# Optimization experiments

Measured on AMD Instinct MI355X. Metric: run time of the kernel, lower is better.

Reference implementation:

```python
import jax, jax.numpy as jnp
import numpy as np

SQRT_2_OVER_PI = 0.7978845608028654

def gelu_tanh(x):
    return 0.5 * x * (1.0 + jnp.tanh(SQRT_2_OVER_PI * (x + 0.044715 * x ** 3)))

def setup_inputs() -> dict:
    key = jax.random.key(0)
    ks = jax.random.split(key, 16)
    B, L, H, Dk, Dv = 4, 512, 8, 64, 64
    dm = H * Dk
    inp = {
        'q': jax.random.normal(ks[0], (B, L, dm), jnp.float32),
        'k': jax.random.normal(ks[1], (B, L, dm), jnp.float32),
        'v': jax.random.normal(ks[2], (B, L, dm), jnp.float32),
        'vec_adj_k': jax.random.normal(ks[3], (B, L, L, Dk), jnp.float32),
        'vec_adj_v': jax.random.normal(ks[4], (B, L, L, Dv), jnp.float32),
        'adj_k': jax.random.randint(ks[5], (B, L, L), 0, 2, jnp.int32),
        'adj_v': jax.random.randint(ks[6], (B, L, L), 0, 2, jnp.int32),
        # learned params (Linear weights stored as [in, out]; y = x @ W)
        'w_qs': jax.random.normal(ks[7], (dm, H * Dk), jnp.float32) * 0.02,
        'w_ks': jax.random.normal(ks[8], (dm, H * Dk), jnp.float32) * 0.02,
        'w_vs': jax.random.normal(ks[9], (dm, H * Dv), jnp.float32) * 0.02,
        'w_fc': jax.random.normal(ks[10], (H * Dk, H * Dk), jnp.float32) * 0.02,
        'w_nw': jax.random.normal(ks[11], (H * Dk, 1), jnp.float32) * 0.02,
        'w_self': jax.random.normal(ks[12], (H * Dk, H * Dk), jnp.float32) * 0.02,
        'w_dd': jax.random.normal(ks[13], (H * Dk, H * Dk), jnp.float32) * 0.02,
    }
    return inp

def reference(q, k, v, vec_adj_k, vec_adj_v, adj_k, adj_v,
              w_qs, w_ks, w_vs, w_fc, w_nw, w_self, w_dd):
    H, Dk, Dv = 8, 64, 64
    B, L, dm = q.shape
    temperature = Dk ** 0.5
    residual = q
    # projections -> [B, H, L, D]
    qh = (q @ w_qs).reshape(B, L, H, Dk).transpose(0, 2, 1, 3)
    kh = (k @ w_ks).reshape(B, L, H, Dk).transpose(0, 2, 1, 3)
    vh = (v @ w_vs).reshape(B, L, H, Dv).transpose(0, 2, 1, 3)
    qs = qh / temperature
    # inner_(q, k, vec_adj_k, flag=True): content + relative-position scores
    scores = jnp.einsum('bhld,bhmd->bhlm', qs, kh) \
           + jnp.einsum('bhld,blmd->bhlm', qs, vec_adj_k)  # [B,H,L,L]
    # adjacency mask (mask == 0 -> -10000)
    scores = jnp.where(adj_k[:, None, :, :] == 0, jnp.float32(-10000.0), scores)
    attn = jax.nn.softmax(scores, axis=-1)
    # inner_(attn, v, vec_adj_v, flag=False)
    out = jnp.einsum('bhlm,bhmd->bhld', attn, vh) \
        + jnp.einsum('bhlm,blmd->bhld', attn, vec_adj_v)
    qc = out.transpose(0, 2, 1, 3).reshape(B, L, H * Dv)  # [B,L,dm]
    # masked neighbor aggregation (GNN stage)
    adj_f = adj_k.astype(qc.dtype)
    nn_num = adj_f.sum(-1)                                  # [B,L]
    denom = jnp.where(nn_num >= 1.0, nn_num, 1.0)
    node_weight = jax.nn.sigmoid((qc @ w_nw)[..., 0])       # [B,L]
    self_info = qc @ w_self
    dd_info = qc @ w_dd
    dd_weight = node_weight[:, None, :] * adj_f             # [B,L,L]
    agg = jnp.matmul(dd_weight, dd_info) / denom[..., None]
    qo = gelu_tanh((self_info + agg) @ w_fc)
    qo = residual + qo
    return (qo, attn)
```

## Files before the change

kernel.cpp:

```cpp
#include <hip/hip_runtime.h>
#include <cstdint>


typedef __attribute__((ext_vector_type(8))) short short8;
typedef __attribute__((ext_vector_type(4))) float f32x4;

__device__ __forceinline__ unsigned short f2bf(float f){
  union { float f; unsigned u; } v; v.f = f;
  unsigned r = (v.u + 0x7fffu + ((v.u >> 16) & 1u)) >> 16;
  return (unsigned short)r;
}

__device__ __forceinline__ short8 ld8(const unsigned short* p){
  return *(const short8*)p;
}

__device__ __forceinline__ f32x4 mfma16(short8 a, short8 b, f32x4 c){
  return __builtin_amdgcn_mfma_f32_16x16x32_bf16(a, b, c, 0, 0, 0);
}

__device__ __forceinline__ float gelu_tanh(float x){
  float u = 0.7978845608028654f * (x + 0.044715f * x * x * x);
  return 0.5f * x * (1.f + tanhf(u));
}

__device__ __forceinline__ short8 pack8(float4 f0, float4 f1){
  short8 s;
  s[0] = (short)f2bf(f0.x); s[1] = (short)f2bf(f0.y);
  s[2] = (short)f2bf(f0.z); s[3] = (short)f2bf(f0.w);
  s[4] = (short)f2bf(f1.x); s[5] = (short)f2bf(f1.y);
  s[6] = (short)f2bf(f1.z); s[7] = (short)f2bf(f1.w);
  return s;
}

template<int LDA, int LDB, int KSTEPS>
__device__ __forceinline__ void gemm64(const unsigned short* __restrict__ A,
                                       const unsigned short* __restrict__ Bp,
                                       f32x4 acc[4][4]){
#pragma unroll 2
  for (int ks = 0; ks < KSTEPS; ks++){
    int kk = ks * 32;
    short8 a[4], b[4];
#pragma unroll
    for (int i = 0; i < 4; i++){
      a[i] = ld8(A + (size_t)i * 16 * LDA + kk);
      b[i] = ld8(Bp + (size_t)i * 16 * LDB + kk);
    }
#pragma unroll
    for (int i = 0; i < 4; i++)
#pragma unroll
      for (int j = 0; j < 4; j++)
        acc[i][j] = mfma16(a[i], b[j], acc[i][j]);
  }
}

__global__ __launch_bounds__(256) void k_prep(const float* __restrict__ q,
    const float* __restrict__ k, const float* __restrict__ v,
    unsigned short* __restrict__ xin,
    const float* __restrict__ wqs, const float* __restrict__ wks,
    const float* __restrict__ wvs, const float* __restrict__ wself,
    const float* __restrict__ wdd, const float* __restrict__ wfc,
    unsigned short* __restrict__ Wt){
  int blk = blockIdx.x;
  int t = threadIdx.x;
  if (blk < 3072){
    int i = blk * 256 + t;
    int w = i >> 18, r = i & 262143;
    const float* src = (w == 0) ? q : (w == 1) ? k : v;
    float4 f = *(const float4*)(src + (size_t)r * 4);
    unsigned lo = (unsigned)f2bf(f.x) | ((unsigned)f2bf(f.y) << 16);
    unsigned hi = (unsigned)f2bf(f.z) | ((unsigned)f2bf(f.w) << 16);
    uint2 o; o.x = lo; o.y = hi;
    *(uint2*)(xin + (size_t)w * 1048576 + (size_t)r * 4) = o;
  } else {
    int i = (blk - 3072) * 256 + t;
    int w = i >> 13;
    int rr = i & 8191;
    int kg = rr >> 9;
    int n  = rr & 511;
    int k0 = kg * 32;
    const float* src = (w == 0) ? wqs : (w == 1) ? wks : (w == 2) ? wvs :
                       (w == 3) ? wself : (w == 4) ? wdd : wfc;
    unsigned pk[16];
#pragma unroll
    for (int j = 0; j < 16; j++){
      float a = src[(size_t)(k0 + 2 * j) * 512 + n];
      float b = src[(size_t)(k0 + 2 * j + 1) * 512 + n];
      pk[j] = (unsigned)f2bf(a) | ((unsigned)f2bf(b) << 16);
    }
    uint4* o4 = (uint4*)(Wt + (size_t)w * 262144 + (size_t)n * 512 + k0);
    o4[0] = make_uint4(pk[0],  pk[1],  pk[2],  pk[3]);
    o4[1] = make_uint4(pk[4],  pk[5],  pk[6],  pk[7]);
    o4[2] = make_uint4(pk[8],  pk[9],  pk[10], pk[11]);
    o4[3] = make_uint4(pk[12], pk[13], pk[14], pk[15]);
  }
}

__global__ __launch_bounds__(256) void k_proj(const unsigned short* __restrict__ xin,
    const unsigned short* __restrict__ Wt, unsigned short* __restrict__ qsb,
    unsigned short* __restrict__ khb, unsigned short* __restrict__ vhT){
  int wid = blockIdx.x * 4 + (threadIdx.x >> 6);
  int mode = wid >> 8;
  int tile = wid & 255;
  int tm = tile >> 3, tn = tile & 7;
  int lane = threadIdx.x & 63;
  int r = lane & 15, qq = lane >> 4;
  const unsigned short* X = xin + (size_t)mode * 1048576;
  const unsigned short* W = Wt + (size_t)mode * 262144;
  unsigned short* dst = (mode == 0) ? qsb : (mode == 1) ? khb : vhT;
  const unsigned short* A  = X + (size_t)(tm * 64 + r) * 512 + qq * 8;
  const unsigned short* Bp = W + (size_t)(tn * 64 + r) * 512 + qq * 8;
  f32x4 acc[4][4] = {};
  gemm64<512, 512, 16>(A, Bp, acc);
  float scv = (mode == 0) ? 0.125f : 1.0f;
  int h = tn;
#pragma unroll
  for (int i = 0; i < 4; i++)
#pragma unroll
    for (int j = 0; j < 4; j++)
#pragma unroll
      for (int e = 0; e < 4; e++){
        int row = tm * 64 + i * 16 + qq * 4 + e;
        int d = j * 16 + r;
        int bb = row >> 9, l = row & 511;
        unsigned short val = f2bf(acc[i][j][e] * scv);
        size_t idx = (mode == 2) ? ((size_t)((bb * 8 + h) * 64 + d) * 512 + l)
                                 : ((size_t)((bb * 8 + h) * 512 + l) * 64 + d);
        dst[idx] = val;
      }
}

__global__ __launch_bounds__(256) void k_scores(const unsigned short* __restrict__ qs,
    const unsigned short* __restrict__ kh, float* __restrict__ attnF){
  int wid = blockIdx.x * 4 + (threadIdx.x >> 6);
  int bh = wid >> 6;
  int tile = wid & 63;
  int tm = tile >> 3, tn = tile & 7;
  int lane = threadIdx.x & 63;
  int r = lane & 15, qq = lane >> 4;
  const unsigned short* A  = qs + (size_t)bh * 32768 + (size_t)(tm * 64 + r) * 64 + qq * 8;
  const unsigned short* Bp = kh + (size_t)bh * 32768 + (size_t)(tn * 64 + r) * 64 + qq * 8;
  f32x4 acc[4][4] = {};
  gemm64<64, 64, 2>(A, Bp, acc);
  float* C = attnF + (size_t)bh * 262144;
#pragma unroll
  for (int i = 0; i < 4; i++)
#pragma unroll
    for (int j = 0; j < 4; j++)
#pragma unroll
      for (int e = 0; e < 4; e++){
        int row = tm * 64 + i * 16 + qq * 4 + e;
        int col = tn * 64 + j * 16 + r;
        C[(size_t)row * 512 + col] = acc[i][j][e];
      }
}

__global__ __launch_bounds__(256) void k_relsoft(const unsigned short* __restrict__ qs,
    const float* __restrict__ vak, const int* __restrict__ adj,
    float* __restrict__ attnF, unsigned short* __restrict__ attn_bf){
  int bid = blockIdx.x;
  int b = bid >> 9, l = bid & 511;
  int t = threadIdx.x, lane = t & 63, w = t >> 6;
  __shared__ __align__(16) unsigned short qsA[16 * 64];
  __shared__ float sc[8 * 512];
  __shared__ int adjs[512];
  for (int j = 0; j < 4; j++){
    int e = t + j * 256;
    int m = e >> 6, d = e & 63;
    qsA[e] = (m < 8) ? qs[((size_t)((b * 8 + m) * 512 + l)) * 64 + d] : (unsigned short)0;
  }
  for (int j = 0; j < 16; j++){
    int e = t + j * 256;
    int h = e >> 9, m = e & 511;
    sc[e] = attnF[((size_t)(b * 8 + h) * 512 + l) * 512 + m];
  }
  adjs[t]       = adj[(size_t)bid * 512 + t];
  adjs[t + 256] = adj[(size_t)bid * 512 + t + 256];
  __syncthreads();
  int r = lane & 15, qq = lane >> 4;
  short8 a0 = ld8(qsA + r * 64 + qq * 8);
  short8 a1 = ld8(qsA + r * 64 + 32 + qq * 8);
  const float* vrow = vak + (size_t)bid * 32768;
#pragma unroll
  for (int c = 0; c < 4; c++){
#pragma unroll
    for (int nt2 = 0; nt2 < 2; nt2++){
      int nt = w * 2 + nt2;
      int m0 = c * 128 + nt * 16 + r;
      const float* p = vrow + (size_t)m0 * 64 + qq * 8;
      float4 f0 = *(const float4*)(p);
      float4 f1 = *(const float4*)(p + 4);
      float4 f2 = *(const float4*)(p + 32);
      float4 f3 = *(const float4*)(p + 36);
      f32x4 acc = {0.f, 0.f, 0.f, 0.f};
      acc = mfma16(a0, pack8(f0, f1), acc);
      acc = mfma16(a1, pack8(f2, f3), acc);
      if (qq < 2){
#pragma unroll
        for (int i = 0; i < 4; i++){
          int h = qq * 4 + i;
          sc[h * 512 + c * 128 + nt * 16 + r] += acc[i];
        }
      }
    }
  }
  __syncthreads();
  for (int hh = 0; hh < 2; hh++){
    int h = w * 2 + hh;
    float v[8]; float mx = -3.0e38f;
    for (int i = 0; i < 8; i++){
      int m = lane + i * 64;
      float s = sc[h * 512 + m];
      if (adjs[m] == 0) s = -10000.0f;
      v[i] = s; mx = fmaxf(mx, s);
    }
    for (int off = 32; off; off >>= 1) mx = fmaxf(mx, __shfl_xor(mx, off, 64));
    float sum = 0.f;
    for (int i = 0; i < 8; i++){ v[i] = __expf(v[i] - mx); sum += v[i]; }
    for (int off = 32; off; off >>= 1) sum += __shfl_xor(sum, off, 64);
    float inv = 1.f / sum;
    size_t base = ((size_t)(b * 8 + h) * 512 + l) * 512;
    for (int i = 0; i < 8; i++){
      int m = lane + i * 64;
      float p2 = v[i] * inv;
      attnF[base + m] = p2;
      attn_bf[base + m] = f2bf(p2);
    }
  }
}

__global__ __launch_bounds__(256) void k_outc(const unsigned short* __restrict__ attn_bf,
    const unsigned short* __restrict__ vhT, float* __restrict__ qc){
  int wid = blockIdx.x * 4 + (threadIdx.x >> 6);
  int bh = wid >> 3;
  int tm = wid & 7;
  int lane = threadIdx.x & 63;
  int r = lane & 15, qq = lane >> 4;
  const unsigned short* A  = attn_bf + (size_t)bh * 262144 + (size_t)(tm * 64 + r) * 512 + qq * 8;
  const unsigned short* Bp = vhT + (size_t)bh * 32768 + (size_t)r * 512 + qq * 8;
  f32x4 acc[4][4] = {};
  gemm64<512, 512, 16>(A, Bp, acc);
  int b = bh >> 3, h = bh & 7;
#pragma unroll
  for (int i = 0; i < 4; i++)
#pragma unroll
    for (int j = 0; j < 4; j++)
#pragma unroll
      for (int e = 0; e < 4; e++){
        int lrow = tm * 64 + i * 16 + qq * 4 + e;
        int d = j * 16 + r;
        qc[(size_t)(b * 512 + lrow) * 512 + h * 64 + d] = acc[i][j][e];
      }
}

__global__ __launch_bounds__(256) void k_outrel(const unsigned short* __restrict__ attn_bf,
    const float* __restrict__ vav, const float* __restrict__ qc,
    const int* __restrict__ adj, const float* __restrict__ wnw,
    unsigned short* __restrict__ qc_bf, float* __restrict__ nw, float* __restrict__ invden){
  int bid = blockIdx.x;
  int b = bid >> 9, l = bid & 511;
  int t = threadIdx.x, lane = t & 63, w = t >> 6;
  __shared__ float orL[512];
  __shared__ float redf[4];
  __shared__ int redi[4];
  int r = lane & 15, qq = lane >> 4;
  int h8 = r & 7;
  const float* vrow = vav + (size_t)bid * 32768;
  const unsigned short* arow = attn_bf + ((size_t)(b * 8 + h8) * 512 + l) * 512;
  f32x4 acc = {0.f, 0.f, 0.f, 0.f};
  int dcol = w * 16 + r;
#pragma unroll
  for (int c = 0; c < 4; c++){
#pragma unroll
    for (int s = 0; s < 4; s++){
      int kk = c * 128 + s * 32;
      short8 av = ld8(arow + kk + qq * 8);
      float fv[8];
#pragma unroll
      for (int j = 0; j < 8; j++)
        fv[j] = vrow[(size_t)(kk + qq * 8 + j) * 64 + dcol];
      short8 bv;
#pragma unroll
      for (int j = 0; j < 8; j++) bv[j] = (short)f2bf(fv[j]);
      acc = mfma16(av, bv, acc);
    }
  }
  if (qq < 2){
#pragma unroll
    for (int i = 0; i < 4; i++){
      int h = qq * 4 + i;
      orL[h * 64 + dcol] = acc[i];
    }
  }
  __syncthreads();
  float part = 0.f; int asum = 0;
  for (int j = 0; j < 2; j++){
    int e = t + j * 256;
    float val = qc[(size_t)bid * 512 + e] + orL[e];
    qc_bf[(size_t)bid * 512 + e] = f2bf(val);
    part += val * wnw[e];
    asum += adj[(size_t)bid * 512 + e];
  }
  for (int off = 32; off; off >>= 1){
    part += __shfl_xor(part, off, 64);
    asum += __shfl_xor(asum, off, 64);
  }
  if (lane == 0){ redf[w] = part; redi[w] = asum; }
  __syncthreads();
  if (t == 0){
    float tot = redf[0] + redf[1] + redf[2] + redf[3];
    int at = redi[0] + redi[1] + redi[2] + redi[3];
    nw[bid] = 1.f / (1.f + __expf(-tot));
    invden[bid] = 1.f / ((at >= 1) ? (float)at : 1.f);
  }
}

__global__ __launch_bounds__(256) void k_post(const unsigned short* __restrict__ qcb,
    const unsigned short* __restrict__ Wself, const unsigned short* __restrict__ Wdd,
    float* __restrict__ selfi, unsigned short* __restrict__ ddT,
    const int* __restrict__ adj, const float* __restrict__ nw,
    const float* __restrict__ invden, unsigned short* __restrict__ ddw){
  int blk = blockIdx.x;
  int t = threadIdx.x;
  if (blk < 128){
    int mode = blk >> 6;
    int wid = (blk & 63) * 4 + (t >> 6);
    int tm = wid >> 3, tn = wid & 7;
    int lane = t & 63;
    int r = lane & 15, qq = lane >> 4;
    const unsigned short* W = mode ? Wdd : Wself;
    const unsigned short* A  = qcb + (size_t)(tm * 64 + r) * 512 + qq * 8;
    const unsigned short* Bp = W + (size_t)(tn * 64 + r) * 512 + qq * 8;
    f32x4 acc[4][4] = {};
    gemm64<512, 512, 16>(A, Bp, acc);
#pragma unroll
    for (int i = 0; i < 4; i++)
#pragma unroll
      for (int j = 0; j < 4; j++)
#pragma unroll
        for (int e = 0; e < 4; e++){
          int row = tm * 64 + i * 16 + qq * 4 + e;
          int col = tn * 64 + j * 16 + r;
          if (mode == 0)
            selfi[(size_t)row * 512 + col] = acc[i][j][e];
          else {
            int bb = row >> 9, m = row & 511;
            ddT[((size_t)(bb * 512 + col)) * 512 + m] = f2bf(acc[i][j][e]);
          }
        }
  } else {
    int i8 = ((blk - 128) * 256 + t) * 8;
    int bb = i8 >> 18, rest = i8 & 262143;
    int l = rest >> 9, m0 = rest & 511;
    int4 a0 = *(const int4*)(adj + i8);
    int4 a1 = *(const int4*)(adj + i8 + 4);
    float id = invden[bb * 512 + l];
    const float* nwb = nw + bb * 512 + m0;
    short8 o;
    o[0] = a0.x ? (short)f2bf(nwb[0] * id) : (short)0;
    o[1] = a0.y ? (short)f2bf(nwb[1] * id) : (short)0;
    o[2] = a0.z ? (short)f2bf(nwb[2] * id) : (short)0;
    o[3] = a0.w ? (short)f2bf(nwb[3] * id) : (short)0;
    o[4] = a1.x ? (short)f2bf(nwb[4] * id) : (short)0;
    o[5] = a1.y ? (short)f2bf(nwb[5] * id) : (short)0;
    o[6] = a1.z ? (short)f2bf(nwb[6] * id) : (short)0;
    o[7] = a1.w ? (short)f2bf(nwb[7] * id) : (short)0;
    *(short8*)(ddw + i8) = o;
  }
}

__global__ __launch_bounds__(256) void k_agg(const unsigned short* __restrict__ ddw,
    const unsigned short* __restrict__ ddT, const float* __restrict__ selfi,
    unsigned short* __restrict__ xbf){
  int wid = blockIdx.x * 4 + (threadIdx.x >> 6);
  int b = wid >> 6;
  int tile = wid & 63;
  int tm = tile >> 3, tn = tile & 7;
  int lane = threadIdx.x & 63;
  int r = lane & 15, qq = lane >> 4;
  const unsigned short* A  = ddw + (size_t)b * 262144 + (size_t)(tm * 64 + r) * 512 + qq * 8;
  const unsigned short* Bp = ddT + (size_t)b * 262144 + (size_t)(tn * 64 + r) * 512 + qq * 8;
  f32x4 acc[4][4] = {};
  gemm64<512, 512, 16>(A, Bp, acc);
#pragma unroll
  for (int i = 0; i < 4; i++)
#pragma unroll
    for (int j = 0; j < 4; j++)
#pragma unroll
      for (int e = 0; e < 4; e++){
        int row = b * 512 + tm * 64 + i * 16 + qq * 4 + e;
        int col = tn * 64 + j * 16 + r;
        float x = acc[i][j][e] + selfi[(size_t)row * 512 + col];
        xbf[(size_t)row * 512 + col] = f2bf(x);
      }
}

__global__ __launch_bounds__(256) void k_fc(const unsigned short* __restrict__ xbf,
    const unsigned short* __restrict__ W, const float* __restrict__ qin,
    float* __restrict__ qo){
  int wid = blockIdx.x * 4 + (threadIdx.x >> 6);
  int tm = wid >> 3, tn = wid & 7;
  int lane = threadIdx.x & 63;
  int r = lane & 15, qq = lane >> 4;
  const unsigned short* A  = xbf + (size_t)(tm * 64 + r) * 512 + qq * 8;
  const unsigned short* Bp = W + (size_t)(tn * 64 + r) * 512 + qq * 8;
  f32x4 acc[4][4] = {};
  gemm64<512, 512, 16>(A, Bp, acc);
#pragma unroll
  for (int i = 0; i < 4; i++)
#pragma unroll
    for (int j = 0; j < 4; j++)
#pragma unroll
      for (int e = 0; e < 4; e++){
        int row = tm * 64 + i * 16 + qq * 4 + e;
        int col = tn * 64 + j * 16 + r;
        qo[(size_t)row * 512 + col] = qin[(size_t)row * 512 + col] + gelu_tanh(acc[i][j][e]);
      }
}

extern "C" void kernel_launch(void* const* d_in, const int* in_sizes, int n_in,
                              void* d_out, int out_size, void* d_ws, size_t ws_size,
                              hipStream_t stream){
  const float* q    = (const float*)d_in[0];
  const float* k    = (const float*)d_in[1];
  const float* v    = (const float*)d_in[2];
  const float* vak  = (const float*)d_in[3];
  const float* vav  = (const float*)d_in[4];
  const int*   adjk = (const int*)d_in[5];
  const float* wqs  = (const float*)d_in[7];
  const float* wks  = (const float*)d_in[8];
  const float* wvs  = (const float*)d_in[9];
  const float* wfc  = (const float*)d_in[10];
  const float* wnw  = (const float*)d_in[11];
  const float* wself= (const float*)d_in[12];
  const float* wdd  = (const float*)d_in[13];

  float* qo    = (float*)d_out;
  float* attnF = qo + 1048576;

  char* p = (char*)d_ws;
  unsigned short* xin   = (unsigned short*)p; p += 6291456;
  unsigned short* Wt    = (unsigned short*)p; p += 3145728;
  unsigned short* qsb   = (unsigned short*)p; p += 2097152;
  unsigned short* khb   = (unsigned short*)p; p += 2097152;
  unsigned short* vhT   = (unsigned short*)p; p += 2097152;
  unsigned short* attnb = (unsigned short*)p; p += 16777216;
  float*          qc    = (float*)p;          p += 4194304;
  unsigned short* qcb   = (unsigned short*)p; p += 2097152;
  float*          nw    = (float*)p;          p += 8192;
  float*          invd  = (float*)p;          p += 8192;
  float*          selfi = (float*)p;          p += 4194304;
  unsigned short* ddT   = (unsigned short*)p; p += 2097152;
  unsigned short* ddw   = (unsigned short*)p; p += 2097152;
  unsigned short* xbf   = (unsigned short*)p; p += 2097152;

  k_prep<<<3264, 256, 0, stream>>>(q, k, v, xin, wqs, wks, wvs, wself, wdd, wfc, Wt);
  k_proj<<<192, 256, 0, stream>>>(xin, Wt, qsb, khb, vhT);
  k_scores<<<512, 256, 0, stream>>>(qsb, khb, attnF);
  k_relsoft<<<2048, 256, 0, stream>>>(qsb, vak, adjk, attnF, attnb);
  k_outc<<<64, 256, 0, stream>>>(attnb, vhT, qc);
  k_outrel<<<2048, 256, 0, stream>>>(attnb, vav, qc, adjk, wnw, qcb, nw, invd);
  k_post<<<640, 256, 0, stream>>>(qcb, Wt + 786432, Wt + 1048576, selfi, ddT,
                                  adjk, nw, invd, ddw);
  k_agg<<<64, 256, 0, stream>>>(ddw, ddT, selfi, xbf);
  k_fc<<<64, 256, 0, stream>>>(xbf, Wt + 1310720, q, qo);
}
```

Before: 708.6 us.

## Skip masked neighbors in relative-position kernels and halve GEMM row tiles

In the relative-score and relative-value kernels, each block now builds a compacted list of unmasked neighbor columns with a prefix scan. It then loads and multiplies only those rows of vec_adj_k and vec_adj_v, which cuts the dominant HBM traffic roughly in half for random 0/1 adjacency. The mask is applied while staging the scores, and the neighbor count is reused for the denominator. Separately, all the small GEMM kernels switch from 64-row to 32-row tiles to double the number of blocks. This adds scan and gather overhead and uses scattered row loads.

```diff
diff --git a/kernel.cpp b/kernel.cpp
--- a/kernel.cpp
+++ b/kernel.cpp
@@ -33,21 +33,20 @@
   return s;
 }
 
-template<int LDA, int LDB, int KSTEPS>
-__device__ __forceinline__ void gemm64(const unsigned short* __restrict__ A,
-                                       const unsigned short* __restrict__ Bp,
-                                       f32x4 acc[4][4]){
+template<int MT, int LDA, int LDB, int KSTEPS>
+__device__ __forceinline__ void gemmT(const unsigned short* __restrict__ A,
+                                      const unsigned short* __restrict__ Bp,
+                                      f32x4 acc[MT][4]){
 #pragma unroll 2
   for (int ks = 0; ks < KSTEPS; ks++){
     int kk = ks * 32;
-    short8 a[4], b[4];
-#pragma unroll
-    for (int i = 0; i < 4; i++){
-      a[i] = ld8(A + (size_t)i * 16 * LDA + kk);
-      b[i] = ld8(Bp + (size_t)i * 16 * LDB + kk);
-    }
-#pragma unroll
-    for (int i = 0; i < 4; i++)
+    short8 a[MT], b[4];
+#pragma unroll
+    for (int i = 0; i < MT; i++) a[i] = ld8(A + (size_t)i * 16 * LDA + kk);
+#pragma unroll
+    for (int j = 0; j < 4; j++)  b[j] = ld8(Bp + (size_t)j * 16 * LDB + kk);
+#pragma unroll
+    for (int i = 0; i < MT; i++)
 #pragma unroll
       for (int j = 0; j < 4; j++)
         acc[i][j] = mfma16(a[i], b[j], acc[i][j]);
@@ -100,27 +99,27 @@
     const unsigned short* __restrict__ Wt, unsigned short* __restrict__ qsb,
     unsigned short* __restrict__ khb, unsigned short* __restrict__ vhT){
   int wid = blockIdx.x * 4 + (threadIdx.x >> 6);
-  int mode = wid >> 8;
-  int tile = wid & 255;
+  int mode = wid >> 9;
+  int tile = wid & 511;
   int tm = tile >> 3, tn = tile & 7;
   int lane = threadIdx.x & 63;
   int r = lane & 15, qq = lane >> 4;
   const unsigned short* X = xin + (size_t)mode * 1048576;
   const unsigned short* W = Wt + (size_t)mode * 262144;
   unsigned short* dst = (mode == 0) ? qsb : (mode == 1) ? khb : vhT;
-  const unsigned short* A  = X + (size_t)(tm * 64 + r) * 512 + qq * 8;
+  const unsigned short* A  = X + (size_t)(tm * 32 + r) * 512 + qq * 8;
   const unsigned short* Bp = W + (size_t)(tn * 64 + r) * 512 + qq * 8;
-  f32x4 acc[4][4] = {};
-  gemm64<512, 512, 16>(A, Bp, acc);
+  f32x4 acc[2][4] = {};
+  gemmT<2, 512, 512, 16>(A, Bp, acc);
   float scv = (mode == 0) ? 0.125f : 1.0f;
   int h = tn;
 #pragma unroll
-  for (int i = 0; i < 4; i++)
+  for (int i = 0; i < 2; i++)
 #pragma unroll
     for (int j = 0; j < 4; j++)
 #pragma unroll
       for (int e = 0; e < 4; e++){
-        int row = tm * 64 + i * 16 + qq * 4 + e;
+        int row = tm * 32 + i * 16 + qq * 4 + e;
         int d = j * 16 + r;
         int bb = row >> 9, l = row & 511;
         unsigned short val = f2bf(acc[i][j][e] * scv);
@@ -141,7 +140,7 @@
   const unsigned short* A  = qs + (size_t)bh * 32768 + (size_t)(tm * 64 + r) * 64 + qq * 8;
   const unsigned short* Bp = kh + (size_t)bh * 32768 + (size_t)(tn * 64 + r) * 64 + qq * 8;
   f32x4 acc[4][4] = {};
-  gemm64<64, 64, 2>(A, Bp, acc);
+  gemmT<4, 64, 64, 2>(A, Bp, acc);
   float* C = attnF + (size_t)bh * 262144;
 #pragma unroll
   for (int i = 0; i < 4; i++)
@@ -163,44 +162,61 @@
   int t = threadIdx.x, lane = t & 63, w = t >> 6;
   __shared__ __align__(16) unsigned short qsA[16 * 64];
   __shared__ float sc[8 * 512];
-  __shared__ int adjs[512];
+  __shared__ short Mlist[512];
+  __shared__ int lds4[4];
   for (int j = 0; j < 4; j++){
     int e = t + j * 256;
     int m = e >> 6, d = e & 63;
     qsA[e] = (m < 8) ? qs[((size_t)((b * 8 + m) * 512 + l)) * 64 + d] : (unsigned short)0;
   }
+  int am0 = adj[(size_t)bid * 512 + t];
+  int am1 = adj[(size_t)bid * 512 + t + 256];
   for (int j = 0; j < 16; j++){
     int e = t + j * 256;
     int h = e >> 9, m = e & 511;
-    sc[e] = attnF[((size_t)(b * 8 + h) * 512 + l) * 512 + m];
-  }
-  adjs[t]       = adj[(size_t)bid * 512 + t];
-  adjs[t + 256] = adj[(size_t)bid * 512 + t + 256];
+    float s = attnF[((size_t)(b * 8 + h) * 512 + l) * 512 + m];
+    int msk = (j & 1) ? am1 : am0;
+    sc[e] = msk ? s : -10000.0f;
+  }
+  int2 av2 = *(const int2*)(adj + (size_t)bid * 512 + 2 * t);
+  int c = av2.x + av2.y;
+  int incl = c;
+  for (int off = 1; off < 64; off <<= 1){
+    int n = __shfl_up(incl, off, 64);
+    if (lane >= off) incl += n;
+  }
+  if (lane == 63) lds4[w] = incl;
+  __syncthreads();
+  int base = 0;
+  for (int i = 0; i < w; i++) base += lds4[i];
+  int cnt = lds4[0] + lds4[1] + lds4[2] + lds4[3];
+  int excl = base + incl - c;
+  if (av2.x){ Mlist[excl] = (short)(2 * t); excl++; }
+  if (av2.y){ Mlist[excl] = (short)(2 * t + 1); }
+  int padded = (cnt + 31) & ~31;
+  for (int i2 = cnt + t; i2 < padded; i2 += 256) Mlist[i2] = 0;
   __syncthreads();
   int r = lane & 15, qq = lane >> 4;
   short8 a0 = ld8(qsA + r * 64 + qq * 8);
   short8 a1 = ld8(qsA + r * 64 + 32 + qq * 8);
   const float* vrow = vak + (size_t)bid * 32768;
-#pragma unroll
-  for (int c = 0; c < 4; c++){
-#pragma unroll
-    for (int nt2 = 0; nt2 < 2; nt2++){
-      int nt = w * 2 + nt2;
-      int m0 = c * 128 + nt * 16 + r;
-      const float* p = vrow + (size_t)m0 * 64 + qq * 8;
-      float4 f0 = *(const float4*)(p);
-      float4 f1 = *(const float4*)(p + 4);
-      float4 f2 = *(const float4*)(p + 32);
-      float4 f3 = *(const float4*)(p + 36);
-      f32x4 acc = {0.f, 0.f, 0.f, 0.f};
-      acc = mfma16(a0, pack8(f0, f1), acc);
-      acc = mfma16(a1, pack8(f2, f3), acc);
-      if (qq < 2){
-#pragma unroll
-        for (int i = 0; i < 4; i++){
-          int h = qq * 4 + i;
-          sc[h * 512 + c * 128 + nt * 16 + r] += acc[i];
-        }
+  int ntiles = (cnt + 15) >> 4;
+  for (int tile = w; tile < ntiles; tile += 4){
+    int gi = tile * 16 + r;
+    int m = Mlist[gi];
+    const float* p = vrow + (size_t)m * 64 + qq * 8;
+    float4 f0 = *(const float4*)(p);
+    float4 f1 = *(const float4*)(p + 4);
+    float4 f2 = *(const float4*)(p + 32);
+    float4 f3 = *(const float4*)(p + 36);
+    f32x4 acc = {0.f, 0.f, 0.f, 0.f};
+    acc = mfma16(a0, pack8(f0, f1), acc);
+    acc = mfma16(a1, pack8(f2, f3), acc);
+    if (qq < 2){
+#pragma unroll
+      for (int i = 0; i < 4; i++){
+        int h = qq * 4 + i;
+        if (gi < cnt) sc[h * 512 + m] += acc[i];
       }
     }
   }
@@ -210,21 +226,19 @@
     float v[8]; float mx = -3.0e38f;
     for (int i = 0; i < 8; i++){
       int m = lane + i * 64;
-      float s = sc[h * 512 + m];
-      if (adjs[m] == 0) s = -10000.0f;
-      v[i] = s; mx = fmaxf(mx, s);
+      v[i] = sc[h * 512 + m]; mx = fmaxf(mx, v[i]);
     }
     for (int off = 32; off; off >>= 1) mx = fmaxf(mx, __shfl_xor(mx, off, 64));
     float sum = 0.f;
     for (int i = 0; i < 8; i++){ v[i] = __expf(v[i] - mx); sum += v[i]; }
     for (int off = 32; off; off >>= 1) sum += __shfl_xor(sum, off, 64);
     float inv = 1.f / sum;
-    size_t base = ((size_t)(b * 8 + h) * 512 + l) * 512;
+    size_t base2 = ((size_t)(b * 8 + h) * 512 + l) * 512;
     for (int i = 0; i < 8; i++){
       int m = lane + i * 64;
       float p2 = v[i] * inv;
-      attnF[base + m] = p2;
-      attn_bf[base + m] = f2bf(p2);
+      attnF[base2 + m] = p2;
+      attn_bf[base2 + m] = f2bf(p2);
     }
   }
 }
@@ -232,22 +246,22 @@
 __global__ __launch_bounds__(256) void k_outc(const unsigned short* __restrict__ attn_bf,
     const unsigned short* __restrict__ vhT, float* __restrict__ qc){
   int wid = blockIdx.x * 4 + (threadIdx.x >> 6);
-  int bh = wid >> 3;
-  int tm = wid & 7;
+  int bh = wid >> 4;
+  int tm = wid & 15;
   int lane = threadIdx.x & 63;
   int r = lane & 15, qq = lane >> 4;
-  const unsigned short* A  = attn_bf + (size_t)bh * 262144 + (size_t)(tm * 64 + r) * 512 + qq * 8;
+  const unsigned short* A  = attn_bf + (size_t)bh * 262144 + (size_t)(tm * 32 + r) * 512 + qq * 8;
   const unsigned short* Bp = vhT + (size_t)bh * 32768 + (size_t)r * 512 + qq * 8;
-  f32x4 acc[4][4] = {};
-  gemm64<512, 512, 16>(A, Bp, acc);
+  f32x4 acc[2][4] = {};
+  gemmT<2, 512, 512, 16>(A, Bp, acc);
   int b = bh >> 3, h = bh & 7;
 #pragma unroll
-  for (int i = 0; i < 4; i++)
+  for (int i = 0; i < 2; i++)
 #pragma unroll
     for (int j = 0; j < 4; j++)
 #pragma unroll
       for (int e = 0; e < 4; e++){
-        int lrow = tm * 64 + i * 16 + qq * 4 + e;
+        int lrow = tm * 32 + i * 16 + qq * 4 + e;
         int d = j * 16 + r;
         qc[(size_t)(b * 512 + lrow) * 512 + h * 64 + d] = acc[i][j][e];
       }
@@ -260,30 +274,68 @@
   int bid = blockIdx.x;
   int b = bid >> 9, l = bid & 511;
   int t = threadIdx.x, lane = t & 63, w = t >> 6;
+  __shared__ __align__(16) unsigned short attnL[8][512];
+  __shared__ __align__(16) unsigned short pAg[8][528];
+  __shared__ short Mlist[512];
   __shared__ float orL[512];
   __shared__ float redf[4];
-  __shared__ int redi[4];
+  __shared__ int lds4[4];
   int r = lane & 15, qq = lane >> 4;
   int h8 = r & 7;
+#pragma unroll
+  for (int h = 0; h < 8; h++){
+    const unsigned short* rowp = attn_bf + (((size_t)(b * 8 + h) * 512 + l) * 512);
+    *(ushort2*)(&attnL[h][2 * t]) = *(const ushort2*)(rowp + 2 * t);
+  }
+  int2 av2 = *(const int2*)(adj + (size_t)bid * 512 + 2 * t);
+  int c = av2.x + av2.y;
+  int incl = c;
+  for (int off = 1; off < 64; off <<= 1){
+    int n = __shfl_up(incl, off, 64);
+    if (lane >= off) incl += n;
+  }
+  if (lane == 63) lds4[w] = incl;
+  __syncthreads();
+  int base = 0;
+  for (int i = 0; i < w; i++) base += lds4[i];
+  int cnt = lds4[0] + lds4[1] + lds4[2] + lds4[3];
+  int excl = base + incl - c;
+  if (av2.x){ Mlist[excl] = (short)(2 * t); excl++; }
+  if (av2.y){ Mlist[excl] = (short)(2 * t + 1); }
+  int cntV = cnt;
+  int padded0 = (cnt + 31) & ~31;
+  for (int i2 = cnt + t; i2 < padded0; i2 += 256) Mlist[i2] = 0;
+  __syncthreads();
+  if (cnt == 0){
+    for (int i2 = t; i2 < 512; i2 += 256) Mlist[i2] = (short)i2;
+    cntV = 512;
+    __syncthreads();
+  }
+  int padded = (cntV + 31) & ~31;
+  for (int j = t; j < padded; j += 256){
+    int m = Mlist[j];
+    bool vld = (j < cntV);
+#pragma unroll
+    for (int h = 0; h < 8; h++)
+      pAg[h][j] = vld ? attnL[h][m] : (unsigned short)0;
+  }
+  __syncthreads();
   const float* vrow = vav + (size_t)bid * 32768;
-  const unsigned short* arow = attn_bf + ((size_t)(b * 8 + h8) * 512 + l) * 512;
+  int dcol = w * 16 + r;
   f32x4 acc = {0.f, 0.f, 0.f, 0.f};
-  int dcol = w * 16 + r;
-#pragma unroll
-  for (int c = 0; c < 4; c++){
-#pragma unroll
-    for (int s = 0; s < 4; s++){
-      int kk = c * 128 + s * 32;
-      short8 av = ld8(arow + kk + qq * 8);
-      float fv[8];
-#pragma unroll
-      for (int j = 0; j < 8; j++)
-        fv[j] = vrow[(size_t)(kk + qq * 8 + j) * 64 + dcol];
-      short8 bv;
-#pragma unroll
-      for (int j = 0; j < 8; j++) bv[j] = (short)f2bf(fv[j]);
-      acc = mfma16(av, bv, acc);
-    }
+  int nks = padded >> 5;
+  for (int s = 0; s < nks; s++){
+    short8 av = ld8(&pAg[h8][s * 32 + qq * 8]);
+    int mrow[8];
+#pragma unroll
+    for (int j = 0; j < 8; j++) mrow[j] = Mlist[s * 32 + qq * 8 + j];
+    float fv[8];
+#pragma unroll
+    for (int j = 0; j < 8; j++) fv[j] = vrow[(size_t)mrow[j] * 64 + dcol];
+    short8 bv;
+#pragma unroll
+    for (int j = 0; j < 8; j++) bv[j] = (short)f2bf(fv[j]);
+    acc = mfma16(av, bv, acc);
   }
   if (qq < 2){
 #pragma unroll
@@ -293,25 +345,20 @@
     }
   }
   __syncthreads();
-  float part = 0.f; int asum = 0;
+  float part = 0.f;
   for (int j = 0; j < 2; j++){
     int e = t + j * 256;
     float val = qc[(size_t)bid * 512 + e] + orL[e];
     qc_bf[(size_t)bid * 512 + e] = f2bf(val);
     part += val * wnw[e];
-    asum += adj[(size_t)bid * 512 + e];
-  }
-  for (int off = 32; off; off >>= 1){
-    part += __shfl_xor(part, off, 64);
-    asum += __shfl_xor(asum, off, 64);
-  }
-  if (lane == 0){ redf[w] = part; redi[w] = asum; }
+  }
+  for (int off = 32; off; off >>= 1) part += __shfl_xor(part, off, 64);
+  if (lane == 0) redf[w] = part;
   __syncthreads();
   if (t == 0){
     float tot = redf[0] + redf[1] + redf[2] + redf[3];
-    int at = redi[0] + redi[1] + redi[2] + redi[3];
     nw[bid] = 1.f / (1.f + __expf(-tot));
-    invden[bid] = 1.f / ((at >= 1) ? (float)at : 1.f);
+    invden[bid] = 1.f / ((cnt >= 1) ? (float)cnt : 1.f);
   }
 }
 
@@ -322,24 +369,24 @@
     const float* __restrict__ invden, unsigned short* __restrict__ ddw){
   int blk = blockIdx.x;
   int t = threadIdx.x;
-  if (blk < 128){
-    int mode = blk >> 6;
-    int wid = (blk & 63) * 4 + (t >> 6);
+  if (blk < 256){
+    int mode = blk >> 7;
+    int wid = (blk & 127) * 4 + (t >> 6);
     int tm = wid >> 3, tn = wid & 7;
     int lane = t & 63;
     int r = lane & 15, qq = lane >> 4;
     const unsigned short* W = mode ? Wdd : Wself;
-    const unsigned short* A  = qcb + (size_t)(tm * 64 + r) * 512 + qq * 8;
+    const unsigned short* A  = qcb + (size_t)(tm * 32 + r) * 512 + qq * 8;
     const unsigned short* Bp = W + (size_t)(tn * 64 + r) * 512 + qq * 8;
-    f32x4 acc[4][4] = {};
-    gemm64<512, 512, 16>(A, Bp, acc);
-#pragma unroll
-    for (int i = 0; i < 4; i++)
+    f32x4 acc[2][4] = {};
+    gemmT<2, 512, 512, 16>(A, Bp, acc);
+#pragma unroll
+    for (int i = 0; i < 2; i++)
 #pragma unroll
       for (int j = 0; j < 4; j++)
 #pragma unroll
         for (int e = 0; e < 4; e++){
-          int row = tm * 64 + i * 16 + qq * 4 + e;
+          int row = tm * 32 + i * 16 + qq * 4 + e;
           int col = tn * 64 + j * 16 + r;
           if (mode == 0)
             selfi[(size_t)row * 512 + col] = acc[i][j][e];
@@ -349,7 +396,7 @@
           }
         }
   } else {
-    int i8 = ((blk - 128) * 256 + t) * 8;
+    int i8 = ((blk - 256) * 256 + t) * 8;
     int bb = i8 >> 18, rest = i8 & 262143;
     int l = rest >> 9, m0 = rest & 511;
     int4 a0 = *(const int4*)(adj + i8);
@@ -373,22 +420,22 @@
     const unsigned short* __restrict__ ddT, const float* __restrict__ selfi,
     unsigned short* __restrict__ xbf){
   int wid = blockIdx.x * 4 + (threadIdx.x >> 6);
-  int b = wid >> 6;
-  int tile = wid & 63;
+  int b = wid >> 7;
+  int tile = wid & 127;
   int tm = tile >> 3, tn = tile & 7;
   int lane = threadIdx.x & 63;
   int r = lane & 15, qq = lane >> 4;
-  const unsigned short* A  = ddw + (size_t)b * 262144 + (size_t)(tm * 64 + r) * 512 + qq * 8;
+  const unsigned short* A  = ddw + (size_t)b * 262144 + (size_t)(tm * 32 + r) * 512 + qq * 8;
   const unsigned short* Bp = ddT + (size_t)b * 262144 + (size_t)(tn * 64 + r) * 512 + qq * 8;
-  f32x4 acc[4][4] = {};
-  gemm64<512, 512, 16>(A, Bp, acc);
-#pragma unroll
-  for (int i = 0; i < 4; i++)
+  f32x4 acc[2][4] = {};
+  gemmT<2, 512, 512, 16>(A, Bp, acc);
+#pragma unroll
+  for (int i = 0; i < 2; i++)
 #pragma unroll
     for (int j = 0; j < 4; j++)
 #pragma unroll
       for (int e = 0; e < 4; e++){
-        int row = b * 512 + tm * 64 + i * 16 + qq * 4 + e;
+        int row = b * 512 + tm * 32 + i * 16 + qq * 4 + e;
         int col = tn * 64 + j * 16 + r;
         float x = acc[i][j][e] + selfi[(size_t)row * 512 + col];
         xbf[(size_t)row * 512 + col] = f2bf(x);
@@ -402,17 +449,17 @@
   int tm = wid >> 3, tn = wid & 7;
   int lane = threadIdx.x & 63;
   int r = lane & 15, qq = lane >> 4;
-  const unsigned short* A  = xbf + (size_t)(tm * 64 + r) * 512 + qq * 8;
+  const unsigned short* A  = xbf + (size_t)(tm * 32 + r) * 512 + qq * 8;
   const unsigned short* Bp = W + (size_t)(tn * 64 + r) * 512 + qq * 8;
-  f32x4 acc[4][4] = {};
-  gemm64<512, 512, 16>(A, Bp, acc);
-#pragma unroll
-  for (int i = 0; i < 4; i++)
+  f32x4 acc[2][4] = {};
+  gemmT<2, 512, 512, 16>(A, Bp, acc);
+#pragma unroll
+  for (int i = 0; i < 2; i++)
 #pragma unroll
     for (int j = 0; j < 4; j++)
 #pragma unroll
       for (int e = 0; e < 4; e++){
-        int row = tm * 64 + i * 16 + qq * 4 + e;
+        int row = tm * 32 + i * 16 + qq * 4 + e;
         int col = tn * 64 + j * 16 + r;
         qo[(size_t)row * 512 + col] = qin[(size_t)row * 512 + col] + gelu_tanh(acc[i][j][e]);
       }
@@ -455,13 +502,13 @@
   unsigned short* xbf   = (unsigned short*)p; p += 2097152;
 
   k_prep<<<3264, 256, 0, stream>>>(q, k, v, xin, wqs, wks, wvs, wself, wdd, wfc, Wt);
-  k_proj<<<192, 256, 0, stream>>>(xin, Wt, qsb, khb, vhT);
+  k_proj<<<384, 256, 0, stream>>>(xin, Wt, qsb, khb, vhT);
   k_scores<<<512, 256, 0, stream>>>(qsb, khb, attnF);
   k_relsoft<<<2048, 256, 0, stream>>>(qsb, vak, adjk, attnF, attnb);
-  k_outc<<<64, 256, 0, stream>>>(attnb, vhT, qc);
+  k_outc<<<128, 256, 0, stream>>>(attnb, vhT, qc);
   k_outrel<<<2048, 256, 0, stream>>>(attnb, vav, qc, adjk, wnw, qcb, nw, invd);
-  k_post<<<640, 256, 0, stream>>>(qcb, Wt + 786432, Wt + 1048576, selfi, ddT,
+  k_post<<<768, 256, 0, stream>>>(qcb, Wt + 786432, Wt + 1048576, selfi, ddT,
                                   adjk, nw, invd, ddw);
-  k_agg<<<64, 256, 0, stream>>>(ddw, ddT, selfi, xbf);
-  k_fc<<<64, 256, 0, stream>>>(xbf, Wt + 1310720, q, qo);
-}
+  k_agg<<<128, 256, 0, stream>>>(ddw, ddT, selfi, xbf);
+  k_fc<<<128, 256, 0, stream>>>(xbf, Wt + 1310720, q, qo);
+}
```

New measurement: 618.9 us. -12.7%, faster.
